# Performance work log

Hardware: AMD Instinct MI355X
Metric: run time of the kernel (lower is better)

## Reference

```python
import jax, jax.numpy as jnp
import numpy as np

NH, NKV, HD = 32, 8, 64
GROUPS = NH // NKV
NLAYERS, FREQ = 30, 3
NSLOTS = 1 + NLAYERS // FREQ  # 11
LAYER_IDX = 0
TOPK = 128
KB_SCALE = 100.0
PAD = -3.3895313892515355e+38  # torch.finfo(bfloat16).min


def rotate_half(x):
    d = x.shape[-1] // 2
    return jnp.concatenate([-x[..., d:], x[..., :d]], axis=-1)


def apply_rope(x, cos, sin):
    # x: (B, H, S, D); cos/sin: (B, S, D)
    return x * cos[:, None] + rotate_half(x) * sin[:, None]


def setup_inputs() -> dict:
    key = jax.random.key(0)
    ks = jax.random.split(key, 10)
    B, S, H = 2, 1024, 2048
    KBL = 400
    hidden_states = jax.random.normal(ks[0], (B, S, H), jnp.float32)
    # rotary embeddings (LlamaRotaryEmbedding, theta=10000)
    pos = jnp.arange(S, dtype=jnp.float32)
    inv_freq = 1.0 / (10000.0 ** (jnp.arange(0, HD, 2, dtype=jnp.float32) / HD))
    freqs = pos[:, None] * inv_freq[None, :]
    emb = jnp.concatenate([freqs, freqs], axis=-1)  # (S, HD)
    cos = jnp.broadcast_to(jnp.cos(emb)[None], (B, S, HD)).astype(jnp.float32)
    sin = jnp.broadcast_to(jnp.sin(emb)[None], (B, S, HD)).astype(jnp.float32)
    # additive causal mask (B,1,S,S)
    causal = jnp.where(jnp.tril(jnp.ones((S, S), jnp.bool_)), 0.0, PAD).astype(jnp.float32)
    attention_mask = jnp.broadcast_to(causal[None, None], (B, 1, S, S))
    kb_keys = jax.random.normal(ks[1], (KBL, NSLOTS * NH * HD), jnp.float32) * 0.5
    kb_values = jax.random.normal(ks[2], (KBL, NSLOTS * NH * HD), jnp.float32) * 0.5
    s = 0.02
    Wq = jax.random.normal(ks[3], (NH * HD, H), jnp.float32) * s
    Wq2 = jax.random.normal(ks[4], (NH * HD, H), jnp.float32) * s
    Wk = jax.random.normal(ks[5], (NKV * HD, H), jnp.float32) * s
    Wv = jax.random.normal(ks[6], (NKV * HD, H), jnp.float32) * s
    Wo = jax.random.normal(ks[7], (H, NH * HD), jnp.float32) * s
    return {"hidden_states": hidden_states, "cos": cos, "sin": sin,
            "attention_mask": attention_mask, "kb_keys": kb_keys, "kb_values": kb_values,
            "Wq": Wq, "Wq2": Wq2, "Wk": Wk, "Wv": Wv, "Wo": Wo}


def reference(hidden_states, cos, sin, attention_mask, kb_keys, kb_values, Wq, Wq2, Wk, Wv, Wo):
    B, S, H = hidden_states.shape
    scale = 1.0 / jnp.sqrt(jnp.float32(HD))

    # projections (attention_bias=False)
    q = (hidden_states @ Wq.T).reshape(B, S, NH, HD).transpose(0, 2, 1, 3)
    q2 = (hidden_states @ Wq2.T).reshape(B, S, NH, HD).transpose(0, 2, 1, 3)
    k = (hidden_states @ Wk.T).reshape(B, S, NKV, HD).transpose(0, 2, 1, 3)
    v = (hidden_states @ Wv.T).reshape(B, S, NKV, HD).transpose(0, 2, 1, 3)

    q = apply_rope(q, cos, sin)
    k = apply_rope(k, cos, sin)

    # repeat_kv (GQA)
    k = jnp.repeat(k, GROUPS, axis=1)  # (B, NH, S, HD)
    v = jnp.repeat(v, GROUPS, axis=1)

    # KB slot select (layer_idx % freq == 0, kb_idx = layer_idx // freq = 0)
    KBL = kb_keys.shape[0]
    kb_idx = LAYER_IDX // FREQ
    kbk = kb_keys.reshape(KBL, NSLOTS, NH * HD)[:, kb_idx].reshape(KBL, NH, HD).transpose(1, 0, 2)
    kbv = kb_values.reshape(KBL, NSLOTS, NH * HD)[:, kb_idx].reshape(KBL, NH, HD).transpose(1, 0, 2)
    kbk = jnp.broadcast_to(kbk[None], (B, NH, KBL, HD))
    kbv = jnp.broadcast_to(kbv[None], (B, NH, KBL, HD))

    # dynamic_sparsify: prune_key_value
    aw_kb = jnp.einsum('bhsd,bhkd->bhsk', q2, kbk) * scale  # (B,NH,S,KBL)
    scores = aw_kb.sum(axis=(1, 2))  # (B, KBL)
    top_idx = jax.lax.stop_gradient(jax.lax.top_k(scores, TOPK)[1])  # (B, TOPK)
    idx = jnp.broadcast_to(top_idx[:, None, :, None], (B, NH, TOPK, HD))
    kbk_g = jax.lax.stop_gradient(jnp.take_along_axis(kbk, idx, axis=2))  # gather under no_grad
    kbv_g = jax.lax.stop_gradient(jnp.take_along_axis(kbv, idx, axis=2))
    aw2 = aw_kb[..., :TOPK]  # source slices (not gathers) the first topk columns

    key_states = jnp.concatenate([kbk_g, k], axis=2)  # (B,NH,TOPK+S,HD)
    value_states = jnp.concatenate([kbv_g, v], axis=2)

    # KB attention mask block
    padding = jnp.all(attention_mask < 0, axis=-1, keepdims=True)  # (B,1,S,1)
    kb_mask = jnp.where(padding, PAD, 0.0).astype(attention_mask.dtype)
    kb_mask = jnp.broadcast_to(kb_mask, (B, 1, S, TOPK))
    mask = jnp.concatenate([kb_mask, attention_mask], axis=-1)  # (B,1,S,TOPK+S)

    aw = jnp.einsum('bhsd,bhkd->bhsk', q, key_states) * scale
    # seperate_query_head: replace KB block with q2-based scores (with kb scale shift)
    aw_seq = aw[..., TOPK:]
    aw2 = aw2 - np.log(TOPK) + np.log(KB_SCALE)
    aw = jnp.concatenate([aw2, aw_seq], axis=-1)

    aw = aw + mask[:, :, :, :key_states.shape[2]]
    aw = jax.nn.softmax(aw.astype(jnp.float32), axis=-1).astype(q.dtype)

    attn = jnp.einsum('bhsk,bhkd->bhsd', aw, value_states)  # (B,NH,S,HD)
    attn = attn.transpose(0, 2, 1, 3).reshape(B, S, NH * HD)
    return attn @ Wo.T
```

## Files before the change

### kernel.cpp

```cpp
#include <hip/hip_runtime.h>
#include <hip/hip_bf16.h>
#include <math.h>

#define NH 32
#define NKV 8
#define HD 64
#define NSLOTS 11
#define TOPK 128
#define KBROW (NSLOTS * NH * HD)
#define PADF (-3.3895313892515355e+38f)
#define C0F  (-0.24686007793152578f)
#define SCALE 0.125f
#define HCH 32

typedef __attribute__((ext_vector_type(8))) __bf16 bf16x8;
typedef __attribute__((ext_vector_type(8))) unsigned short u16x8;
typedef __attribute__((ext_vector_type(4))) float f32x4;

#define GLDS16(gp, lp)                                                        \
  __builtin_amdgcn_global_load_lds(                                           \
      (__attribute__((address_space(1))) void*)(gp),                          \
      (__attribute__((address_space(3))) void*)(lp), 16, 0, 0)

__device__ __forceinline__ unsigned short f2bf(float f) {
  unsigned int u = __float_as_uint(f);
  u = (u + 0x7fffu + ((u >> 16) & 1u)) >> 16;
  return (unsigned short)u;
}

__device__ __forceinline__ int swz(int row, int chunk) {
  return row * 128 + ((chunk ^ (row & 7)) << 4);
}

__global__ void f2bf_kernel(const float* __restrict__ in,
                            unsigned short* __restrict__ out, int n4) {
  int i = blockIdx.x * blockDim.x + threadIdx.x;
  if (i >= n4) return;
  float4 v = ((const float4*)in)[i];
  ushort4 o;
  o.x = f2bf(v.x); o.y = f2bf(v.y); o.z = f2bf(v.z); o.w = f2bf(v.w);
  ((ushort4*)out)[i] = o;
}

__global__ void f2bf4_kernel(const float* __restrict__ s0,
                             const float* __restrict__ s1,
                             const float* __restrict__ s2,
                             const float* __restrict__ s3,
                             int n0, int n1, int n2, int n3,
                             unsigned short* __restrict__ out) {
  int i = blockIdx.x * blockDim.x + threadIdx.x;
  int j = i;
  const float* src;
  if (j < n0) src = s0;
  else {
    j -= n0;
    if (j < n1) src = s1;
    else {
      j -= n1;
      if (j < n2) src = s2;
      else {
        j -= n2;
        if (j >= n3) return;
        src = s3;
      }
    }
  }
  float4 v = ((const float4*)src)[j];
  ushort4 o = {f2bf(v.x), f2bf(v.y), f2bf(v.z), f2bf(v.w)};
  ((ushort4*)out)[i] = o;
}

__global__ __launch_bounds__(256) void gemm_nt_bf16(
    const unsigned short* __restrict__ A, const unsigned short* __restrict__ B,
    float* __restrict__ C, int M, int N, int K) {
  __shared__ unsigned short ldsA[128 * 32];
  __shared__ unsigned short ldsB[128 * 32];
  const int t = threadIdx.x;
  const int l = t & 63, w = t >> 6;
  const int wr = w >> 1, wc = w & 1;
  const int lr = l & 15;
  const int kb = (l >> 4) * 16;
  const int bm = blockIdx.y * 128, bn = blockIdx.x * 128;

  f32x4 acc[4][4] = {};

  for (int k0 = 0; k0 < K; k0 += 32) {
    __syncthreads();
#pragma unroll
    for (int it = 0; it < 2; ++it) {
      int s = it * 256 + t;
      int row = s >> 2, cs = (s & 3) * 8;
      GLDS16(A + (size_t)(bm + row) * K + k0 + cs,
             (char*)ldsA + (it * 4 + w) * 1024);
      GLDS16(B + (size_t)(bn + row) * K + k0 + cs,
             (char*)ldsB + (it * 4 + w) * 1024);
    }
    __syncthreads();

    bf16x8 a[4], b[4];
#pragma unroll
    for (int m = 0; m < 4; ++m)
      a[m] = *(const bf16x8*)((const char*)ldsA +
                              (wr * 64 + m * 16 + lr) * 64 + kb);
#pragma unroll
    for (int n = 0; n < 4; ++n)
      b[n] = *(const bf16x8*)((const char*)ldsB +
                              (wc * 64 + n * 16 + lr) * 64 + kb);
#pragma unroll
    for (int m = 0; m < 4; ++m)
#pragma unroll
      for (int n = 0; n < 4; ++n)
        acc[m][n] =
            __builtin_amdgcn_mfma_f32_16x16x32_bf16(a[m], b[n], acc[m][n], 0, 0, 0);
  }

#pragma unroll
  for (int m = 0; m < 4; ++m)
#pragma unroll
    for (int n = 0; n < 4; ++n) {
      int rbase = bm + wr * 64 + m * 16 + ((l >> 4) << 2);
      int cbase = bn + wc * 64 + n * 16 + lr;
#pragma unroll
      for (int j = 0; j < 4; ++j)
        C[(size_t)(rbase + j) * N + cbase] = acc[m][n][j];
    }
}

__global__ __launch_bounds__(256) void gemm_proj(
    const unsigned short* __restrict__ A, const unsigned short* __restrict__ Wall,
    const float* __restrict__ cosb, const float* __restrict__ sinb,
    unsigned short* __restrict__ qbf, unsigned short* __restrict__ q2bf,
    unsigned short* __restrict__ kbf, float* __restrict__ vb, int M, int K) {
  __shared__ unsigned short ldsA[128 * 32];
  __shared__ unsigned short ldsB[128 * 32];
  const int t = threadIdx.x;
  const int l = t & 63, w = t >> 6;
  const int wr = w >> 1, wc = w & 1;
  const int lr = l & 15;
  const int kb_ = (l >> 4) * 16;
  const int bm = blockIdx.y * 128, bn = blockIdx.x * 128;

  f32x4 acc[4][4] = {};

  for (int k0 = 0; k0 < K; k0 += 32) {
    __syncthreads();
#pragma unroll
    for (int it = 0; it < 2; ++it) {
      int s = it * 256 + t;
      int row = s >> 2, cs = (s & 3) * 8;
      GLDS16(A + (size_t)(bm + row) * K + k0 + cs,
             (char*)ldsA + (it * 4 + w) * 1024);
      GLDS16(Wall + (size_t)(bn + row) * K + k0 + cs,
             (char*)ldsB + (it * 4 + w) * 1024);
    }
    __syncthreads();

    bf16x8 a[4], b[4];
#pragma unroll
    for (int m = 0; m < 4; ++m)
      a[m] = *(const bf16x8*)((const char*)ldsA +
                              (wr * 64 + m * 16 + lr) * 64 + kb_);
#pragma unroll
    for (int n = 0; n < 4; ++n)
      b[n] = *(const bf16x8*)((const char*)ldsB +
                              (wc * 64 + n * 16 + lr) * 64 + kb_);
#pragma unroll
    for (int m = 0; m < 4; ++m)
#pragma unroll
      for (int n = 0; n < 4; ++n)
        acc[m][n] =
            __builtin_amdgcn_mfma_f32_16x16x32_bf16(a[m], b[n], acc[m][n], 0, 0, 0);
  }

#pragma unroll
  for (int m = 0; m < 4; ++m) {
    int rbase = bm + wr * 64 + m * 16 + ((l >> 4) << 2);
    if (bn < 2048 || (bn >= 4096 && bn < 4608)) {
      const bool isq = bn < 2048;
#pragma unroll
      for (int j = 0; j < 4; ++j) {
        int row = rbase + j;
        const float* cr = cosb + (size_t)row * 64;
        const float* sr = sinb + (size_t)row * 64;
        float c0 = cr[lr], c1 = cr[16 + lr], c2 = cr[32 + lr], c3 = cr[48 + lr];
        float sa = sr[lr], sb = sr[16 + lr], sc_ = sr[32 + lr], sd = sr[48 + lr];
        float x0 = acc[m][0][j], x1 = acc[m][1][j];
        float x2 = acc[m][2][j], x3 = acc[m][3][j];
        float y0 = x0 * c0 - x2 * sa;
        float y1 = x1 * c1 - x3 * sb;
        float y2 = x2 * c2 + x0 * sc_;
        float y3 = x3 * c3 + x1 * sd;
        if (isq) {
          size_t ro = (size_t)row * 2048 + bn + wc * 64 + lr;
          qbf[ro] = f2bf(y0); qbf[ro + 16] = f2bf(y1);
          qbf[ro + 32] = f2bf(y2); qbf[ro + 48] = f2bf(y3);
        } else {
          size_t ro = (size_t)row * 512 + (bn - 4096) + wc * 64 + lr;
          kbf[ro] = f2bf(y0); kbf[ro + 16] = f2bf(y1);
          kbf[ro + 32] = f2bf(y2); kbf[ro + 48] = f2bf(y3);
        }
      }
    } else if (bn < 4096) {
#pragma unroll
      for (int n = 0; n < 4; ++n) {
        int cbase = bn + wc * 64 + n * 16 + lr;
#pragma unroll
        for (int j = 0; j < 4; ++j)
          q2bf[(size_t)(rbase + j) * 2048 + (cbase - 2048)] = f2bf(acc[m][n][j]);
      }
    } else {
#pragma unroll
      for (int n = 0; n < 4; ++n) {
        int cbase = bn + wc * 64 + n * 16 + lr;
#pragma unroll
        for (int j = 0; j < 4; ++j)
          vb[(size_t)(rbase + j) * 512 + (cbase - 4608)] = acc[m][n][j];
      }
    }
  }
}

__global__ __launch_bounds__(256) void vT_kernel(
    const float* __restrict__ vbuf, unsigned short* __restrict__ vT,
    int B, int S) {
  const int nst = S >> 6;
  int stile = blockIdx.x % nst;
  int g = (blockIdx.x / nst) % NKV;
  int b = blockIdx.x / (nst * NKV);
  int s0 = stile * 64;
  __shared__ float lt[64][68];
  int t = threadIdx.x;
#pragma unroll
  for (int it = 0; it < 4; ++it) {
    int slot = it * 256 + t;
    int sl = slot >> 4, d4 = (slot & 15) * 4;
    float4 v = *(const float4*)&vbuf[((size_t)(b * S + s0 + sl) * NKV + g) * 64 + d4];
    lt[sl][d4] = v.x; lt[sl][d4 + 1] = v.y; lt[sl][d4 + 2] = v.z; lt[sl][d4 + 3] = v.w;
  }
  __syncthreads();
#pragma unroll
  for (int it = 0; it < 2; ++it) {
    int slot = it * 256 + t;
    int d = slot >> 3, s8 = (slot & 7) * 8;
    u16x8 o;
#pragma unroll
    for (int j = 0; j < 8; ++j) o[j] = f2bf(lt[s8 + j][d]);
    *(u16x8*)&vT[(((size_t)b * NKV + g) * 64 + d) * S + s0 + s8] = o;
  }
}

__global__ void kbkh_kernel(const float* __restrict__ kbk,
                            unsigned short* __restrict__ out) {
  int i = blockIdx.x * blockDim.x + threadIdx.x;
  if (i >= 128 * 512) return;
  int j = i >> 9, c4 = (i & 511) * 4;
  float4 v = *(const float4*)&kbk[(size_t)j * KBROW + c4];
  ushort4 o = {f2bf(v.x), f2bf(v.y), f2bf(v.z), f2bf(v.w)};
  *(ushort4*)&out[(size_t)j * 2048 + c4] = o;
}

__global__ __launch_bounds__(256) void kbvgt_kernel(
    const float* __restrict__ kbv, const int* __restrict__ topi,
    unsigned short* __restrict__ kbvgT, int B) {
  int h = blockIdx.x % NH, b = blockIdx.x / NH;
  __shared__ unsigned short gt[128][72];
  __shared__ int lidx[TOPK];
  int t = threadIdx.x;
  if (t < TOPK) lidx[t] = topi[b * TOPK + t];
  __syncthreads();
#pragma unroll
  for (int it = 0; it < 8; ++it) {
    int slot = it * 256 + t;
    int j = slot >> 4, d4 = (slot & 15) * 4;
    float4 v = *(const float4*)&kbv[(size_t)lidx[j] * KBROW + h * 64 + d4];
    gt[j][d4] = f2bf(v.x); gt[j][d4 + 1] = f2bf(v.y);
    gt[j][d4 + 2] = f2bf(v.z); gt[j][d4 + 3] = f2bf(v.w);
  }
  __syncthreads();
#pragma unroll
  for (int it = 0; it < 4; ++it) {
    int slot = it * 256 + t;
    int d = slot >> 4, j8 = (slot & 15) * 8;
    u16x8 o;
#pragma unroll
    for (int j = 0; j < 8; ++j) o[j] = gt[j8 + j][d];
    *(u16x8*)&kbvgT[(((size_t)b * NH + h) * 64 + d) * 128 + j8] = o;
  }
}

__global__ __launch_bounds__(256) void hsum1_kernel(
    const float* __restrict__ hidden, double* __restrict__ part,
    int B, int S, int H) {
  const int nhb = H >> 8;
  int hb = blockIdx.x % nhb;
  int ch = (blockIdx.x / nhb) % HCH;
  int b  = blockIdx.x / (nhb * HCH);
  int c  = hb * 256 + threadIdx.x;
  int rows = S / HCH;
  const float* p = hidden + ((size_t)b * S + (size_t)ch * rows) * H + c;
  double acc = 0.0;
  for (int s = 0; s < rows; ++s) acc += (double)p[(size_t)s * H];
  part[((size_t)b * HCH + ch) * H + c] = acc;
}

__global__ void hsum2_kernel(const double* __restrict__ part,
                             float* __restrict__ Hsum, int B, int H) {
  int idx = blockIdx.x * blockDim.x + threadIdx.x;
  if (idx >= B * H) return;
  int b = idx / H, c = idx % H;
  const double* p = part + (size_t)b * HCH * H + c;
  double acc = 0.0;
#pragma unroll
  for (int ch = 0; ch < HCH; ++ch) acc += p[(size_t)ch * H];
  Hsum[idx] = (float)acc;
}

__global__ void qs_kernel(const float* __restrict__ Hsum,
                          const float* __restrict__ Wq2,
                          float* __restrict__ Qs, int B, int H) {
  int task = (blockIdx.x * blockDim.x + threadIdx.x) >> 6;
  int lane = threadIdx.x & 63;
  if (task >= B * NH * HD) return;
  int b = task / (NH * HD), c = task % (NH * HD);
  const float* hs = Hsum + (size_t)b * H;
  const float* wr = Wq2 + (size_t)c * H;
  double acc = 0.0;
  for (int k = lane; k < H; k += 64) acc += (double)hs[k] * (double)wr[k];
#pragma unroll
  for (int off = 32; off; off >>= 1) acc += __shfl_xor(acc, off);
  if (lane == 0) Qs[task] = (float)acc;
}

__global__ void scores_kernel(const float* __restrict__ Qs,
                              const float* __restrict__ kbk,
                              float* __restrict__ scores, int B, int KBL) {
  int task = (blockIdx.x * blockDim.x + threadIdx.x) >> 6;
  int lane = threadIdx.x & 63;
  if (task >= B * KBL) return;
  int b = task / KBL, l = task % KBL;
  const float* kr = kbk + (size_t)l * KBROW;
  const float* qd = Qs + (size_t)b * NH * HD;
  double acc = 0.0;
  for (int c = lane; c < NH * HD; c += 64) acc += (double)qd[c] * (double)kr[c];
#pragma unroll
  for (int off = 32; off; off >>= 1) acc += __shfl_xor(acc, off);
  if (lane == 0) scores[task] = (float)(0.125 * acc);
}

__global__ __launch_bounds__(256) void topk_kernel(
    const float* __restrict__ scores, int* __restrict__ top_idx, int KBL) {
  __shared__ float ls[512];
  int b = blockIdx.x, t = threadIdx.x;
  for (int i = t; i < KBL; i += 256) ls[i] = scores[(size_t)b * KBL + i];
  __syncthreads();
  for (int l = t; l < KBL; l += 256) {
    float sl = ls[l];
    int rank = 0;
    for (int j = 0; j < KBL; ++j) {
      float sj = ls[j];
      rank += (sj > sl || (sj == sl && j < l)) ? 1 : 0;
    }
    if (rank < TOPK) top_idx[b * TOPK + rank] = l;
  }
}

__global__ void padflag_kernel(const float* __restrict__ mask,
                               int* __restrict__ flags, int BS, int S) {
  int w = (blockIdx.x * blockDim.x + threadIdx.x) >> 6;
  int lane = threadIdx.x & 63;
  if (w >= BS) return;
  const float* row = mask + (size_t)w * S;
  bool ok = true;
  for (int j = lane; j < S; j += 64) ok = ok && (row[j] < 0.f);
  int allv = __all(ok ? 1 : 0);
  if (lane == 0) flags[w] = allv;
}

__device__ __forceinline__ void attn_step(
    const char* smem, char* ptw, const int* padfb, const bf16x8* aq,
    bool iskb, int j0, int s0, int w, int li, int lg4,
    float* m_, float* l_, f32x4* acc) {
  f32x4 cc[4];
  __builtin_amdgcn_s_setprio(1);
#pragma unroll
  for (int cb = 0; cb < 4; ++cb) {
    bf16x8 b0 = *(const bf16x8*)(smem + swz(cb * 16 + li, lg4));
    bf16x8 b1 = *(const bf16x8*)(smem + swz(cb * 16 + li, 4 + lg4));
    f32x4 z = {};
    z = __builtin_amdgcn_mfma_f32_16x16x32_bf16(aq[0], b0, z, 0, 0, 0);
    z = __builtin_amdgcn_mfma_f32_16x16x32_bf16(aq[1], b1, z, 0, 0, 0);
    cc[cb] = z;
  }
  __builtin_amdgcn_s_setprio(0);

  float lgv[4][4];
#pragma unroll
  for (int cb = 0; cb < 4; ++cb)
#pragma unroll
    for (int j = 0; j < 4; ++j) {
      float v = SCALE * cc[cb][j];
      if (iskb) {
        v += C0F + (padfb[w * 16 + lg4 * 4 + j] ? PADF : 0.f);
      } else {
        int key = j0 + cb * 16 + li;
        int srow = s0 + w * 16 + lg4 * 4 + j;
        v += (key <= srow) ? 0.f : PADF;
      }
      lgv[cb][j] = v;
    }
#pragma unroll
  for (int j = 0; j < 4; ++j) {
    float rmax = fmaxf(fmaxf(lgv[0][j], lgv[1][j]), fmaxf(lgv[2][j], lgv[3][j]));
#pragma unroll
    for (int off = 8; off; off >>= 1) rmax = fmaxf(rmax, __shfl_xor(rmax, off));
    float mn = fmaxf(m_[j], rmax);
    float fs = __expf(m_[j] - mn);
    float csum = 0.f;
#pragma unroll
    for (int cb = 0; cb < 4; ++cb) {
      float pv = __expf(lgv[cb][j] - mn);
      csum += pv;
      int key = cb * 16 + li;
      int rloc = lg4 * 4 + j;
      *(unsigned short*)(ptw + swz(rloc, key >> 3) + ((key & 7) << 1)) = f2bf(pv);
    }
#pragma unroll
    for (int off = 8; off; off >>= 1) csum += __shfl_xor(csum, off);
    m_[j] = mn;
    l_[j] = l_[j] * fs + csum;
#pragma unroll
    for (int db = 0; db < 4; ++db) acc[db][j] *= fs;
  }

  bf16x8 pa0 = *(const bf16x8*)(ptw + swz(li, lg4));
  bf16x8 pa1 = *(const bf16x8*)(ptw + swz(li, 4 + lg4));
  __builtin_amdgcn_s_setprio(1);
#pragma unroll
  for (int db = 0; db < 4; ++db) {
    bf16x8 bv0 = *(const bf16x8*)(smem + 8192 + swz(db * 16 + li, lg4));
    bf16x8 bv1 = *(const bf16x8*)(smem + 8192 + swz(db * 16 + li, 4 + lg4));
    acc[db] = __builtin_amdgcn_mfma_f32_16x16x32_bf16(pa0, bv0, acc[db], 0, 0, 0);
    acc[db] = __builtin_amdgcn_mfma_f32_16x16x32_bf16(pa1, bv1, acc[db], 0, 0, 0);
  }
  __builtin_amdgcn_s_setprio(0);
}

__global__ __launch_bounds__(256) void attn_mfma(
    const unsigned short* __restrict__ qbf,
    const unsigned short* __restrict__ q2bf,
    const unsigned short* __restrict__ kbf,
    const unsigned short* __restrict__ vTb,
    const unsigned short* __restrict__ kbkh,
    const unsigned short* __restrict__ kbvgT,
    const int* __restrict__ padflag,
    unsigned short* __restrict__ attnbf,
    int B, int S) {
  const int nst = S >> 6;
  const int npair = (nst + 1) >> 1;
  const int p = blockIdx.x % npair;
  const int h = (blockIdx.x / npair) % NH;
  const int b = blockIdx.x / (npair * NH);
  const int stA = p, stB = nst - 1 - p;
  const bool hasB = (stB != stA);
  const int s0A = stA * 64, s0B = stB * 64;
  const int g = h / (NH / NKV);

  __shared__ unsigned short smem[8192];
  __shared__ unsigned short pt[4][1024];
  __shared__ int padf[128];

  const int t = threadIdx.x;
  const int w = t >> 6;
  const int li = t & 15;
  const int lg4 = (t & 63) >> 4;

  if (t < 64) padf[t] = padflag[b * S + s0A + t];
  else if (t < 128) padf[t] = padflag[b * S + s0B + (t - 64)];

  bf16x8 aq0A[2], aq2A[2], aq0B[2], aq2B[2];
#pragma unroll
  for (int pass = 0; pass < 2; ++pass) {
    int s0 = pass ? s0B : s0A;
#pragma unroll
    for (int it = 0; it < 4; ++it) {
      int slot = it * 256 + t;
      int tile = slot >> 9, row = (slot >> 3) & 63, ck = slot & 7;
      const unsigned short* src = tile ? q2bf : qbf;
      bf16x8 v = *(const bf16x8*)(src + (size_t)(b * S + s0 + row) * (NH * HD) +
                                  h * 64 + ck * 8);
      *(bf16x8*)((char*)smem + tile * 8192 + swz(row, ck)) = v;
    }
    __syncthreads();
#pragma unroll
    for (int kc = 0; kc < 2; ++kc) {
      bf16x8 v0 = *(const bf16x8*)((char*)smem + swz(w * 16 + li, kc * 4 + lg4));
      bf16x8 v2 = *(const bf16x8*)((char*)smem + 8192 + swz(w * 16 + li, kc * 4 + lg4));
      if (pass == 0) { aq0A[kc] = v0; aq2A[kc] = v2; }
      else           { aq0B[kc] = v0; aq2B[kc] = v2; }
    }
    __syncthreads();
  }

  float mA[4] = {-3.4e38f, -3.4e38f, -3.4e38f, -3.4e38f};
  float mB[4] = {-3.4e38f, -3.4e38f, -3.4e38f, -3.4e38f};
  float lA[4] = {}, lB[4] = {};
  f32x4 accA[4] = {}, accB[4] = {};

  const int nch = 2 + stB + 1;
  for (int ch = 0; ch < nch; ++ch) {
    const bool iskb = ch < 2;
    const int j0 = iskb ? ch * 64 : (ch - 2) * 64;
    if (ch) __syncthreads();
#pragma unroll
    for (int it = 0; it < 4; ++it) {
      int slot = it * 256 + t;
      int tile = slot >> 9, row = (slot >> 3) & 63, ck = slot & 7;
      const unsigned short* src;
      if (tile == 0) {
        src = iskb ? kbkh + (size_t)(j0 + row) * 2048 + h * 64 + ck * 8
                   : kbf + (size_t)(b * S + j0 + row) * 512 + g * 64 + ck * 8;
      } else {
        src = iskb ? kbvgT + (((size_t)b * NH + h) * 64 + row) * 128 + j0 + ck * 8
                   : vTb + (((size_t)b * NKV + g) * 64 + row) * (size_t)S + j0 + ck * 8;
      }
      bf16x8 v = *(const bf16x8*)src;
      *(bf16x8*)((char*)smem + tile * 8192 + swz(row, ck)) = v;
    }
    __syncthreads();

    if (iskb || (ch - 2) <= stA)
      attn_step((const char*)smem, (char*)pt[w], padf, iskb ? aq2A : aq0A,
                iskb, j0, s0A, w, li, lg4, mA, lA, accA);
    if (hasB)
      attn_step((const char*)smem, (char*)pt[w], padf + 64, iskb ? aq2B : aq0B,
                iskb, j0, s0B, w, li, lg4, mB, lB, accB);
  }

#pragma unroll
  for (int j = 0; j < 4; ++j) {
    float inv = 1.f / lA[j];
    size_t o = (size_t)(b * S + s0A + w * 16 + lg4 * 4 + j) * (NH * HD) + h * 64 + li;
#pragma unroll
    for (int db = 0; db < 4; ++db) attnbf[o + db * 16] = f2bf(accA[db][j] * inv);
  }
  if (hasB) {
#pragma unroll
    for (int j = 0; j < 4; ++j) {
      float inv = 1.f / lB[j];
      size_t o = (size_t)(b * S + s0B + w * 16 + lg4 * 4 + j) * (NH * HD) + h * 64 + li;
#pragma unroll
      for (int db = 0; db < 4; ++db) attnbf[o + db * 16] = f2bf(accB[db][j] * inv);
    }
  }
}

extern "C" void kernel_launch(void* const* d_in, const int* in_sizes, int n_in,
                              void* d_out, int out_size, void* d_ws, size_t ws_size,
                              hipStream_t stream) {
  const float* hidden = (const float*)d_in[0];
  const float* cosb   = (const float*)d_in[1];
  const float* sinb   = (const float*)d_in[2];
  const float* mask   = (const float*)d_in[3];
  const float* kbk    = (const float*)d_in[4];
  const float* kbv    = (const float*)d_in[5];
  const float* Wq     = (const float*)d_in[6];
  const float* Wq2    = (const float*)d_in[7];
  const float* Wk     = (const float*)d_in[8];
  const float* Wv     = (const float*)d_in[9];
  const float* Wo     = (const float*)d_in[10];
  float* out = (float*)d_out;

  const int H   = in_sizes[6] / (NH * HD);
  const int KBL = in_sizes[4] / KBROW;
  const long long BSll = (long long)in_sizes[0] / H;
  const int S = (int)((long long)in_sizes[3] / BSll);
  const int B = (int)(BSll / S);
  const int BS = B * S;
  const int NQ = NH * HD;
  const int NKVD = NKV * HD;
  const int NTOT = NQ + NQ + NKVD + NKVD;

  float* ws = (float*)d_ws;
  size_t off = 0;
  double* hpart = (double*)(ws + off); off += (size_t)B * HCH * H * 2;
  float* vb   = ws + off; off += (size_t)BS * NKVD;
  float* Hsum = ws + off; off += (size_t)B * H;
  float* Qs   = ws + off; off += (size_t)B * NQ;
  float* sc   = ws + off; off += (size_t)B * KBL;
  int* topi   = (int*)(ws + off); off += (size_t)B * TOPK;
  int* padfl  = (int*)(ws + off); off += (size_t)BS;
  unsigned short* hbf    = (unsigned short*)(ws + off); off += (size_t)BS * H / 2;
  unsigned short* wall   = (unsigned short*)(ws + off); off += (size_t)NTOT * H / 2;
  unsigned short* wobf   = (unsigned short*)(ws + off); off += (size_t)H * NQ / 2;
  unsigned short* attnbf = (unsigned short*)(ws + off); off += (size_t)BS * NQ / 2;
  unsigned short* qbf    = (unsigned short*)(ws + off); off += (size_t)BS * NQ / 2;
  unsigned short* q2bf   = (unsigned short*)(ws + off); off += (size_t)BS * NQ / 2;
  unsigned short* kbf    = (unsigned short*)(ws + off); off += (size_t)BS * NKVD / 2;
  unsigned short* vTb    = (unsigned short*)(ws + off); off += (size_t)BS * NKVD / 2;
  unsigned short* kbkh   = (unsigned short*)(ws + off); off += (size_t)128 * NQ / 2;
  unsigned short* kbvgT  = (unsigned short*)(ws + off); off += (size_t)B * NH * HD * TOPK / 2;
  (void)ws_size; (void)n_in; (void)out_size;

  {
    int n = BS * H / 4;
    f2bf_kernel<<<(n + 255) / 256, 256, 0, stream>>>(hidden, hbf, n);
    int n0 = NQ * H / 4, n1 = NQ * H / 4, n2 = NKVD * H / 4, n3 = NKVD * H / 4;
    int ntot = n0 + n1 + n2 + n3;
    f2bf4_kernel<<<(ntot + 255) / 256, 256, 0, stream>>>(
        Wq, Wq2, Wk, Wv, n0, n1, n2, n3, wall);
    n = H * NQ / 4;
    f2bf_kernel<<<(n + 255) / 256, 256, 0, stream>>>(Wo, wobf, n);
  }

  gemm_proj<<<dim3(NTOT / 128, BS / 128), 256, 0, stream>>>(
      hbf, wall, cosb, sinb, qbf, q2bf, kbf, vb, BS, H);

  vT_kernel<<<B * NKV * (S / 64), 256, 0, stream>>>(vb, vTb, B, S);

  hsum1_kernel<<<B * HCH * (H / 256), 256, 0, stream>>>(hidden, hpart, B, S, H);
  hsum2_kernel<<<(B * H + 255) / 256, 256, 0, stream>>>(hpart, Hsum, B, H);
  qs_kernel<<<(B * NQ * 64 + 255) / 256, 256, 0, stream>>>(Hsum, Wq2, Qs, B, H);
  scores_kernel<<<(B * KBL * 64 + 255) / 256, 256, 0, stream>>>(Qs, kbk, sc, B, KBL);
  topk_kernel<<<B, 256, 0, stream>>>(sc, topi, KBL);
  padflag_kernel<<<(BS * 64 + 255) / 256, 256, 0, stream>>>(mask, padfl, BS, S);

  kbkh_kernel<<<(128 * 512 + 255) / 256, 256, 0, stream>>>(kbk, kbkh);
  kbvgt_kernel<<<B * NH, 256, 0, stream>>>(kbv, topi, kbvgT, B);

  {
    int nst = S / 64;
    int npair = (nst + 1) / 2;
    attn_mfma<<<B * NH * npair, 256, 0, stream>>>(
        qbf, q2bf, kbf, vTb, kbkh, kbvgT, padfl, attnbf, B, S);
  }

  gemm_nt_bf16<<<dim3(H / 128, BS / 128), 256, 0, stream>>>(attnbf, wobf, out, BS, H, NQ);
}
```

Baseline: 282.3 us.

## Fuse casts, write V transposed in projection, prefetch attention chunks, split-K output GEMM

```diff
diff --git a/kernel.cpp b/kernel.cpp
--- a/kernel.cpp
+++ b/kernel.cpp
@@ -32,47 +32,28 @@
   return row * 128 + ((chunk ^ (row & 7)) << 4);
 }
 
-__global__ void f2bf_kernel(const float* __restrict__ in,
-                            unsigned short* __restrict__ out, int n4) {
-  int i = blockIdx.x * blockDim.x + threadIdx.x;
-  if (i >= n4) return;
-  float4 v = ((const float4*)in)[i];
-  ushort4 o;
-  o.x = f2bf(v.x); o.y = f2bf(v.y); o.z = f2bf(v.z); o.w = f2bf(v.w);
-  ((ushort4*)out)[i] = o;
-}
-
-__global__ void f2bf4_kernel(const float* __restrict__ s0,
-                             const float* __restrict__ s1,
-                             const float* __restrict__ s2,
-                             const float* __restrict__ s3,
-                             int n0, int n1, int n2, int n3,
-                             unsigned short* __restrict__ out) {
+__global__ void f2bf_all(const float* __restrict__ s0, const float* __restrict__ s1,
+                         const float* __restrict__ s2, const float* __restrict__ s3,
+                         const float* __restrict__ s4, const float* __restrict__ s5,
+                         int n0, int n1, int n2, int n3, int n4_, int n5,
+                         unsigned short* __restrict__ out) {
   int i = blockIdx.x * blockDim.x + threadIdx.x;
   int j = i;
   const float* src;
   if (j < n0) src = s0;
-  else {
-    j -= n0;
-    if (j < n1) src = s1;
-    else {
-      j -= n1;
-      if (j < n2) src = s2;
-      else {
-        j -= n2;
-        if (j >= n3) return;
-        src = s3;
-      }
-    }
-  }
+  else { j -= n0; if (j < n1) src = s1;
+  else { j -= n1; if (j < n2) src = s2;
+  else { j -= n2; if (j < n3) src = s3;
+  else { j -= n3; if (j < n4_) src = s4;
+  else { j -= n4_; if (j >= n5) return; src = s5; }}}}}
   float4 v = ((const float4*)src)[j];
   ushort4 o = {f2bf(v.x), f2bf(v.y), f2bf(v.z), f2bf(v.w)};
   ((ushort4*)out)[i] = o;
 }
 
-__global__ __launch_bounds__(256) void gemm_nt_bf16(
+__global__ __launch_bounds__(256) void gemm_nt_splitk(
     const unsigned short* __restrict__ A, const unsigned short* __restrict__ B,
-    float* __restrict__ C, int M, int N, int K) {
+    float* __restrict__ C0, float* __restrict__ C1, int M, int N, int K) {
   __shared__ unsigned short ldsA[128 * 32];
   __shared__ unsigned short ldsB[128 * 32];
   const int t = threadIdx.x;
@@ -81,10 +62,13 @@
   const int lr = l & 15;
   const int kb = (l >> 4) * 16;
   const int bm = blockIdx.y * 128, bn = blockIdx.x * 128;
+  float* C = blockIdx.z ? C1 : C0;
+  const int k0base = blockIdx.z * (K >> 1);
+  const int kend = k0base + (K >> 1);
 
   f32x4 acc[4][4] = {};
 
-  for (int k0 = 0; k0 < K; k0 += 32) {
+  for (int k0 = k0base; k0 < kend; k0 += 32) {
     __syncthreads();
 #pragma unroll
     for (int it = 0; it < 2; ++it) {
@@ -126,11 +110,21 @@
     }
 }
 
+__global__ void add2_kernel(const float* __restrict__ a,
+                            const float* __restrict__ b,
+                            float* __restrict__ o, int n4) {
+  int i = blockIdx.x * blockDim.x + threadIdx.x;
+  if (i >= n4) return;
+  float4 x = ((const float4*)a)[i], y = ((const float4*)b)[i];
+  ((float4*)o)[i] = make_float4(x.x + y.x, x.y + y.y, x.z + y.z, x.w + y.w);
+}
+
 __global__ __launch_bounds__(256) void gemm_proj(
     const unsigned short* __restrict__ A, const unsigned short* __restrict__ Wall,
     const float* __restrict__ cosb, const float* __restrict__ sinb,
     unsigned short* __restrict__ qbf, unsigned short* __restrict__ q2bf,
-    unsigned short* __restrict__ kbf, float* __restrict__ vb, int M, int K) {
+    unsigned short* __restrict__ kbf, unsigned short* __restrict__ vTb,
+    int M, int K, int S) {
   __shared__ unsigned short ldsA[128 * 32];
   __shared__ unsigned short ldsB[128 * 32];
   const int t = threadIdx.x;
@@ -209,43 +203,16 @@
           q2bf[(size_t)(rbase + j) * 2048 + (cbase - 2048)] = f2bf(acc[m][n][j]);
       }
     } else {
+      int b_ = rbase / S, s = rbase % S;
 #pragma unroll
       for (int n = 0; n < 4; ++n) {
-        int cbase = bn + wc * 64 + n * 16 + lr;
-#pragma unroll
-        for (int j = 0; j < 4; ++j)
-          vb[(size_t)(rbase + j) * 512 + (cbase - 4608)] = acc[m][n][j];
+        int col = (bn - 4608) + wc * 64 + n * 16 + lr;
+        int gg = col >> 6, d = col & 63;
+        ushort4 o = {f2bf(acc[m][n][0]), f2bf(acc[m][n][1]),
+                     f2bf(acc[m][n][2]), f2bf(acc[m][n][3])};
+        *(ushort4*)&vTb[(((size_t)b_ * NKV + gg) * 64 + d) * S + s] = o;
       }
     }
-  }
-}
-
-__global__ __launch_bounds__(256) void vT_kernel(
-    const float* __restrict__ vbuf, unsigned short* __restrict__ vT,
-    int B, int S) {
-  const int nst = S >> 6;
-  int stile = blockIdx.x % nst;
-  int g = (blockIdx.x / nst) % NKV;
-  int b = blockIdx.x / (nst * NKV);
-  int s0 = stile * 64;
-  __shared__ float lt[64][68];
-  int t = threadIdx.x;
-#pragma unroll
-  for (int it = 0; it < 4; ++it) {
-    int slot = it * 256 + t;
-    int sl = slot >> 4, d4 = (slot & 15) * 4;
-    float4 v = *(const float4*)&vbuf[((size_t)(b * S + s0 + sl) * NKV + g) * 64 + d4];
-    lt[sl][d4] = v.x; lt[sl][d4 + 1] = v.y; lt[sl][d4 + 2] = v.z; lt[sl][d4 + 3] = v.w;
-  }
-  __syncthreads();
-#pragma unroll
-  for (int it = 0; it < 2; ++it) {
-    int slot = it * 256 + t;
-    int d = slot >> 3, s8 = (slot & 7) * 8;
-    u16x8 o;
-#pragma unroll
-    for (int j = 0; j < 8; ++j) o[j] = f2bf(lt[s8 + j][d]);
-    *(u16x8*)&vT[(((size_t)b * NKV + g) * 64 + d) * S + s0 + s8] = o;
   }
 }
 
@@ -374,6 +341,28 @@
   for (int j = lane; j < S; j += 64) ok = ok && (row[j] < 0.f);
   int allv = __all(ok ? 1 : 0);
   if (lane == 0) flags[w] = allv;
+}
+
+__device__ __forceinline__ void load_chunk(
+    int ch, int t, int b, int h, int g, int S,
+    const unsigned short* __restrict__ kbf, const unsigned short* __restrict__ vTb,
+    const unsigned short* __restrict__ kbkh, const unsigned short* __restrict__ kbvgT,
+    bf16x8* st) {
+  bool iskb = ch < 2;
+  int j0 = iskb ? ch * 64 : (ch - 2) * 64;
+#pragma unroll
+  for (int it = 0; it < 4; ++it) {
+    int slot = it * 256 + t;
+    int tile = slot >> 9, row = (slot >> 3) & 63, ck = slot & 7;
+    const unsigned short* src;
+    if (tile == 0)
+      src = iskb ? kbkh + (size_t)(j0 + row) * 2048 + h * 64 + ck * 8
+                 : kbf + (size_t)(b * S + j0 + row) * 512 + g * 64 + ck * 8;
+    else
+      src = iskb ? kbvgT + (((size_t)b * NH + h) * 64 + row) * 128 + j0 + ck * 8
+                 : vTb + (((size_t)b * NKV + g) * 64 + row) * (size_t)S + j0 + ck * 8;
+    st[it] = *(const bf16x8*)src;
+  }
 }
 
 __device__ __forceinline__ void attn_step(
@@ -474,39 +463,32 @@
   const int li = t & 15;
   const int lg4 = (t & 63) >> 4;
 
+  const int nch = 2 + stB + 1;
+
+  bf16x8 st[4];
+  load_chunk(0, t, b, h, g, S, kbf, vTb, kbkh, kbvgT, st);
+
+  bf16x8 aq0A[2], aq2A[2], aq0B[2], aq2B[2];
+  {
+    size_t rowA = (size_t)(b * S + s0A + w * 16 + li) * (NH * HD);
+    size_t rowB = (size_t)(b * S + s0B + w * 16 + li) * (NH * HD);
+#pragma unroll
+    for (int kc = 0; kc < 2; ++kc) {
+      size_t o = h * 64 + kc * 32 + lg4 * 8;
+      aq0A[kc] = *(const bf16x8*)(qbf + rowA + o);
+      aq2A[kc] = *(const bf16x8*)(q2bf + rowA + o);
+      aq0B[kc] = *(const bf16x8*)(qbf + rowB + o);
+      aq2B[kc] = *(const bf16x8*)(q2bf + rowB + o);
+    }
+  }
   if (t < 64) padf[t] = padflag[b * S + s0A + t];
   else if (t < 128) padf[t] = padflag[b * S + s0B + (t - 64)];
-
-  bf16x8 aq0A[2], aq2A[2], aq0B[2], aq2B[2];
-#pragma unroll
-  for (int pass = 0; pass < 2; ++pass) {
-    int s0 = pass ? s0B : s0A;
-#pragma unroll
-    for (int it = 0; it < 4; ++it) {
-      int slot = it * 256 + t;
-      int tile = slot >> 9, row = (slot >> 3) & 63, ck = slot & 7;
-      const unsigned short* src = tile ? q2bf : qbf;
-      bf16x8 v = *(const bf16x8*)(src + (size_t)(b * S + s0 + row) * (NH * HD) +
-                                  h * 64 + ck * 8);
-      *(bf16x8*)((char*)smem + tile * 8192 + swz(row, ck)) = v;
-    }
-    __syncthreads();
-#pragma unroll
-    for (int kc = 0; kc < 2; ++kc) {
-      bf16x8 v0 = *(const bf16x8*)((char*)smem + swz(w * 16 + li, kc * 4 + lg4));
-      bf16x8 v2 = *(const bf16x8*)((char*)smem + 8192 + swz(w * 16 + li, kc * 4 + lg4));
-      if (pass == 0) { aq0A[kc] = v0; aq2A[kc] = v2; }
-      else           { aq0B[kc] = v0; aq2B[kc] = v2; }
-    }
-    __syncthreads();
-  }
 
   float mA[4] = {-3.4e38f, -3.4e38f, -3.4e38f, -3.4e38f};
   float mB[4] = {-3.4e38f, -3.4e38f, -3.4e38f, -3.4e38f};
   float lA[4] = {}, lB[4] = {};
   f32x4 accA[4] = {}, accB[4] = {};
 
-  const int nch = 2 + stB + 1;
   for (int ch = 0; ch < nch; ++ch) {
     const bool iskb = ch < 2;
     const int j0 = iskb ? ch * 64 : (ch - 2) * 64;
@@ -515,18 +497,10 @@
     for (int it = 0; it < 4; ++it) {
       int slot = it * 256 + t;
       int tile = slot >> 9, row = (slot >> 3) & 63, ck = slot & 7;
-      const unsigned short* src;
-      if (tile == 0) {
-        src = iskb ? kbkh + (size_t)(j0 + row) * 2048 + h * 64 + ck * 8
-                   : kbf + (size_t)(b * S + j0 + row) * 512 + g * 64 + ck * 8;
-      } else {
-        src = iskb ? kbvgT + (((size_t)b * NH + h) * 64 + row) * 128 + j0 + ck * 8
-                   : vTb + (((size_t)b * NKV + g) * 64 + row) * (size_t)S + j0 + ck * 8;
-      }
-      bf16x8 v = *(const bf16x8*)src;
-      *(bf16x8*)((char*)smem + tile * 8192 + swz(row, ck)) = v;
+      *(bf16x8*)((char*)smem + tile * 8192 + swz(row, ck)) = st[it];
     }
     __syncthreads();
+    if (ch + 1 < nch) load_chunk(ch + 1, t, b, h, g, S, kbf, vTb, kbkh, kbvgT, st);
 
     if (iskb || (ch - 2) <= stA)
       attn_step((const char*)smem, (char*)pt[w], padf, iskb ? aq2A : aq0A,
@@ -583,7 +557,6 @@
   float* ws = (float*)d_ws;
   size_t off = 0;
   double* hpart = (double*)(ws + off); off += (size_t)B * HCH * H * 2;
-  float* vb   = ws + off; off += (size_t)BS * NKVD;
   float* Hsum = ws + off; off += (size_t)B * H;
   float* Qs   = ws + off; off += (size_t)B * NQ;
   float* sc   = ws + off; off += (size_t)B * KBL;
@@ -599,23 +572,20 @@
   unsigned short* vTb    = (unsigned short*)(ws + off); off += (size_t)BS * NKVD / 2;
   unsigned short* kbkh   = (unsigned short*)(ws + off); off += (size_t)128 * NQ / 2;
   unsigned short* kbvgT  = (unsigned short*)(ws + off); off += (size_t)B * NH * HD * TOPK / 2;
+  float* c0 = (float*)qbf;
+  float* c1 = (float*)wall;
   (void)ws_size; (void)n_in; (void)out_size;
 
   {
-    int n = BS * H / 4;
-    f2bf_kernel<<<(n + 255) / 256, 256, 0, stream>>>(hidden, hbf, n);
-    int n0 = NQ * H / 4, n1 = NQ * H / 4, n2 = NKVD * H / 4, n3 = NKVD * H / 4;
-    int ntot = n0 + n1 + n2 + n3;
-    f2bf4_kernel<<<(ntot + 255) / 256, 256, 0, stream>>>(
-        Wq, Wq2, Wk, Wv, n0, n1, n2, n3, wall);
-    n = H * NQ / 4;
-    f2bf_kernel<<<(n + 255) / 256, 256, 0, stream>>>(Wo, wobf, n);
+    int n0 = BS * H / 4, n1 = NQ * H / 4, n2 = NQ * H / 4;
+    int n3 = NKVD * H / 4, n4_ = NKVD * H / 4, n5 = H * NQ / 4;
+    int ntot = n0 + n1 + n2 + n3 + n4_ + n5;
+    f2bf_all<<<(ntot + 255) / 256, 256, 0, stream>>>(
+        hidden, Wq, Wq2, Wk, Wv, Wo, n0, n1, n2, n3, n4_, n5, hbf);
   }
 
   gemm_proj<<<dim3(NTOT / 128, BS / 128), 256, 0, stream>>>(
-      hbf, wall, cosb, sinb, qbf, q2bf, kbf, vb, BS, H);
-
-  vT_kernel<<<B * NKV * (S / 64), 256, 0, stream>>>(vb, vTb, B, S);
+      hbf, wall, cosb, sinb, qbf, q2bf, kbf, vTb, BS, H, S);
 
   hsum1_kernel<<<B * HCH * (H / 256), 256, 0, stream>>>(hidden, hpart, B, S, H);
   hsum2_kernel<<<(B * H + 255) / 256, 256, 0, stream>>>(hpart, Hsum, B, H);
@@ -634,5 +604,7 @@
         qbf, q2bf, kbf, vTb, kbkh, kbvgT, padfl, attnbf, B, S);
   }
 
-  gemm_nt_bf16<<<dim3(H / 128, BS / 128), 256, 0, stream>>>(attnbf, wobf, out, BS, H, NQ);
-}
+  gemm_nt_splitk<<<dim3(H / 128, BS / 128, 2), 256, 0, stream>>>(
+      attnbf, wobf, c0, c1, BS, H, NQ);
+  add2_kernel<<<(BS * H / 4 + 255) / 256, 256, 0, stream>>>(c0, c1, out, BS * H / 4);
+}
```

Result: faster. 265.2 us (-6.1%).
